# Kernel optimization log

Measured on AMD Instinct MI355X. Metric: run time of the kernel, lower is better.

The kernel has to match this reference:

```python
import jax, jax.numpy as jnp
import numpy as np

EPS = 1e-5  # torch BatchNorm2d default
Q_SHIFT = 2.0 ** 10   # deci_w = 10
Q_UPPER = 2.0 ** 15   # 2**(deci_w + inte_w) with inte_w = 5


def quantize(a):
    # emulate torch: (a*shift).int() truncates toward zero, clamp, rescale
    q = jnp.trunc(a * Q_SHIFT)
    q = jnp.clip(q, -Q_UPPER, Q_UPPER)
    return q / Q_SHIFT


def bn_train(x, gamma, beta):
    # training-mode BatchNorm2d: biased batch stats over (N, T, V)
    m = x.mean(axis=(0, 2, 3), keepdims=True)
    v = x.var(axis=(0, 2, 3), keepdims=True)
    return (x - m) * jax.lax.rsqrt(v + EPS) * gamma[None, :, None, None] + beta[None, :, None, None]


def setup_inputs() -> dict:
    key = jax.random.key(0)
    ks = jax.random.split(key, 8)
    N, C, T, V, S, K = 64, 64, 300, 25, 3, 9
    x = jax.random.normal(ks[0], (N, C, T, V), jnp.float32)
    A = jax.random.uniform(ks[1], (S, V, V), jnp.float32)
    PA = jax.random.normal(ks[2], (S, V, V), jnp.float32) * 1e-6
    # conv_d: 1x1 convs, (subset, out_ch, in_ch); conv_branch_init scale
    Wd = jax.random.normal(ks[3], (S, C, C), jnp.float32) * np.sqrt(2.0 / (C * S)).astype(np.float32)
    bd = jax.random.normal(ks[4], (S, C), jnp.float32) * 0.01
    gamma1 = jnp.ones((C,), jnp.float32)
    beta1 = jnp.zeros((C,), jnp.float32)
    # temporal 9x1 conv (out_ch, in_ch, K)
    Wt = jax.random.normal(ks[5], (C, C, K), jnp.float32) * np.sqrt(2.0 / (C * K)).astype(np.float32)
    bt = jnp.zeros((C,), jnp.float32)
    gamma2 = jnp.ones((C,), jnp.float32)
    beta2 = jnp.zeros((C,), jnp.float32)
    return {"x": x, "A": A, "PA": PA, "Wd": Wd, "bd": bd,
            "gamma1": gamma1, "beta1": beta1,
            "Wt": Wt, "bt": bt, "gamma2": gamma2, "beta2": beta2}


def reference(x, A, PA, Wd, bd, gamma1, beta1, Wt, bt, gamma2, beta2):
    # --- unit_gcn (prune_switch path, serial<=0, use_ck=False) ---
    Aq = jax.lax.stop_gradient(quantize(A + PA))  # quantize runs under no_grad
    num_subset = A.shape[0]
    z = None
    for s in range(num_subset):  # fixed small structural loop (3 subsets)
        xa = jnp.einsum('nctv,vw->nctw', x, Aq[s])          # graph matmul over V
        zs = jnp.einsum('nctv,oc->notv', xa, Wd[s]) + bd[s][None, :, None, None]  # 1x1 conv
        z = zs if z is None else z + zs
    y = bn_train(z, gamma1, beta1) + x  # down is identity (in==out)
    y = jax.nn.relu(y)
    # --- unit_tcn: 9x1 temporal conv, pad 4, stride 1, then BN ---
    out = jax.lax.conv_general_dilated(
        y, Wt[..., None], window_strides=(1, 1), padding=((4, 4), (0, 0)),
        dimension_numbers=('NCHW', 'OIHW', 'NCHW')) + bt[None, :, None, None]
    out = bn_train(out, gamma2, beta2)
    # --- residual (identity) + ReLU ---
    return jax.nn.relu(out + x)
```

## Files before the change

### kernel.cpp

```cpp
#include <hip/hip_runtime.h>

#define NB 64
#define CB 64
#define TB 300
#define VB 25
#define SB 3
#define KB 9
#define NCNTF 480000.0f

#define WS_SUM1 0
#define WS_SQ1  64
#define WS_SC1  128
#define WS_SH1  192
#define WS_SUM2 256
#define WS_SQ2  320
#define WS_SC2  384
#define WS_SH2  448
#define WS_WTP_BYTE 2048
#define WS_AQP_BYTE 75776
#define WS_WDP_BYTE 88064
#define WS_TC_BYTE  262144
#define ZP_ELEMS    30720000

typedef __attribute__((ext_vector_type(8))) short short8v;
typedef __attribute__((ext_vector_type(4))) float f32x4;
typedef __attribute__((ext_vector_type(16))) float f32x16;

__device__ __forceinline__ float bf2f(unsigned short u) {
  unsigned int v = ((unsigned int)u) << 16;
  float f; __builtin_memcpy(&f, &v, 4); return f;
}
__device__ __forceinline__ unsigned short f2bf(float f) {
  unsigned int x; __builtin_memcpy(&x, &f, 4);
  x += 0x7fffu + ((x >> 16) & 1u);
  return (unsigned short)(x >> 16);
}

__global__ void k0_prep(const float* __restrict__ A, const float* __restrict__ PA,
                        const float* __restrict__ Wd, const float* __restrict__ Wt,
                        float* __restrict__ ws) {
  int gid = blockIdx.x * 256 + threadIdx.x;
  int gs  = gridDim.x * 256;
  for (int i = gid; i < 512; i += gs) ws[i] = 0.f;
  unsigned short* wtp = (unsigned short*)((char*)ws + WS_WTP_BYTE);
  for (int idx = gid; idx < 36*2*64*8; idx += gs) {
    int j = idx & 7, li = (idx >> 3) & 63, mt = (idx >> 9) & 1, kt = idx >> 10;
    int o = mt*32 + (li & 31);
    int i = (kt & 3)*16 + (li >> 5)*8 + j;
    int tap = kt >> 2;
    wtp[idx] = f2bf(Wt[(o*64 + i)*9 + tap]);
  }
  unsigned short* aqp = (unsigned short*)((char*)ws + WS_AQP_BYTE);
  for (int idx = gid; idx < 12*64*8; idx += gs) {
    int j = idx & 7, l = (idx >> 3) & 63, fi = idx >> 9;
    int h = fi & 1, wt = (fi >> 1) & 1, s = fi >> 2;
    int v = (l >> 4)*8 + j, w = wt*16 + (l & 15);
    unsigned short out = 0;
    if (v < VB && w < VB) {
      int ai = (s*VB + v)*VB + w;
      float a = A[ai] + PA[ai];
      float q = truncf(a * 1024.f);
      q = fminf(fmaxf(q, -32768.f), 32768.f);
      float aq = q * (1.f/1024.f);
      unsigned short hi = f2bf(aq);
      out = h ? f2bf(aq - bf2f(hi)) : hi;
    }
    aqp[idx] = out;
  }
  unsigned short* wdp = (unsigned short*)((char*)ws + WS_WDP_BYTE);
  for (int idx = gid; idx < 48*64*8; idx += gs) {
    int j = idx & 7, l = (idx >> 3) & 63, fi = idx >> 9;
    int mt = fi & 3, q2 = fi >> 2;
    int kt = q2 % 6, h = q2 / 6;
    int k = kt*32 + (l >> 4)*8 + j;
    int s = k >> 6, c = k & 63, o = mt*16 + (l & 15);
    float wv = Wd[(s*64 + o)*64 + c];
    unsigned short hi = f2bf(wv);
    wdp[idx] = h ? f2bf(wv - bf2f(hi)) : hi;
  }
}

__global__ __launch_bounds__(512, 4) void k1_gcn(
    const float* __restrict__ x, const float* __restrict__ bd,
    const float* __restrict__ ws, float* __restrict__ wstat,
    unsigned short* __restrict__ zout, unsigned short* __restrict__ xtout)
{
  __shared__ __align__(16) char k1lds[52000];
  __shared__ float s_sum[CB], s_sq[CB];
  unsigned short* xtl = (unsigned short*)k1lds;
  char*  xab = k1lds + 26400;
  float* zg  = (float*)k1lds;
  int tid = threadIdx.x;
  int t0 = blockIdx.x * 8;
  int n  = blockIdx.y;
  int wv = tid >> 6, l = tid & 63, r = l & 15, g = l >> 4;
  int lim = 7500 - t0*25; if (lim > 200) lim = 200;

  if (tid < CB) { s_sum[tid] = 0.f; s_sq[tid] = 0.f; }

  for (int idx4 = tid; idx4 < 3200; idx4 += 512) {
    int c = idx4 / 50, q = idx4 - c*50;
    int tv0 = q*4;
    if (tv0 + 4 <= lim) {
      float4 xv = *(const float4*)(x + (size_t)(n*64 + c)*7500 + t0*25 + tv0);
      xtl[(tv0+0)*66 + c] = f2bf(xv.x);
      xtl[(tv0+1)*66 + c] = f2bf(xv.y);
      xtl[(tv0+2)*66 + c] = f2bf(xv.z);
      xtl[(tv0+3)*66 + c] = f2bf(xv.w);
    }
  }
  __syncthreads();

  short8v b1[4];
  #pragma unroll
  for (int ct = 0; ct < 4; ++ct) {
    int c = ct*16 + r;
    #pragma unroll
    for (int j = 0; j < 8; ++j) {
      int v = g*8 + j;
      b1[ct][j] = (v < VB) ? (short)xtl[(wv*25 + v)*66 + c] : (short)0;
    }
  }
  for (int idx = tid; idx < 12800; idx += 512) {
    int tv = idx >> 6, c = idx & 63;
    if (tv < lim)
      xtout[n*480000 + t0*1600 + idx] = xtl[tv*66 + c];
  }

  const unsigned short* aqp = (const unsigned short*)((const char*)ws + WS_AQP_BYTE);
  const unsigned short* wdp = (const unsigned short*)((const char*)ws + WS_WDP_BYTE);
  int mt2 = wv & 3, th2 = wv >> 2;
  f32x4 acc2[7];
  #pragma unroll
  for (int i = 0; i < 7; ++i) acc2[i] = (f32x4){0.f,0.f,0.f,0.f};

  for (int s = 0; s < SB; ++s) {
    #pragma unroll
    for (int wt = 0; wt < 2; ++wt) {
      short8v a1h = *(const short8v*)(aqp + ((s*4 + wt*2 + 0)*64 + l)*8);
      short8v a1l = *(const short8v*)(aqp + ((s*4 + wt*2 + 1)*64 + l)*8);
      f32x4 acc1[4];
      #pragma unroll
      for (int ct = 0; ct < 4; ++ct) acc1[ct] = (f32x4){0.f,0.f,0.f,0.f};
      #pragma unroll
      for (int ct = 0; ct < 4; ++ct) {
        acc1[ct] = __builtin_amdgcn_mfma_f32_16x16x32_bf16(a1h, b1[ct], acc1[ct], 0,0,0);
        acc1[ct] = __builtin_amdgcn_mfma_f32_16x16x32_bf16(a1l, b1[ct], acc1[ct], 0,0,0);
      }
      #pragma unroll
      for (int ct = 0; ct < 4; ++ct)
        #pragma unroll
        for (int reg = 0; reg < 4; ++reg) {
          int w = wt*16 + g*4 + reg;
          if (w < VB) {
            int row = wv*25 + w, c = ct*16 + r;
            int bir = (c*2) ^ ((row & 7) << 4);
            *(unsigned short*)(xab + row*128 + bir) = f2bf(acc1[ct][reg]);
          }
        }
    }
    __syncthreads();
    #pragma unroll
    for (int ktl = 0; ktl < 2; ++ktl) {
      int kt = s*2 + ktl;
      short8v ah = *(const short8v*)(wdp + ((kt*4 + mt2)*64 + l)*8);
      short8v al = *(const short8v*)(wdp + (((6 + kt)*4 + mt2)*64 + l)*8);
      #pragma unroll
      for (int ctl = 0; ctl < 7; ++ctl) {
        int rowb = th2*112 + ctl*16 + r;
        if (rowb > 199) rowb = 199;
        int bir = (ktl*64 + g*16) ^ ((rowb & 7) << 4);
        short8v b = *(const short8v*)(xab + rowb*128 + bir);
        acc2[ctl] = __builtin_amdgcn_mfma_f32_16x16x32_bf16(ah, b, acc2[ctl], 0,0,0);
        acc2[ctl] = __builtin_amdgcn_mfma_f32_16x16x32_bf16(al, b, acc2[ctl], 0,0,0);
      }
    }
    __syncthreads();
  }

  #pragma unroll
  for (int ctl = 0; ctl < 7; ++ctl) {
    int tw = th2*112 + ctl*16 + r;
    if (tw < 200) {
      #pragma unroll
      for (int reg = 0; reg < 4; ++reg)
        zg[tw*65 + mt2*16 + g*4 + reg] = acc2[ctl][reg];
    }
  }
  __syncthreads();

  {
    int o = tid & 63, chunk = tid >> 6;
    float bsum = bd[o] + bd[CB + o] + bd[2*CB + o];
    unsigned short* zr = zout + n*480000 + t0*1600 + o;
    float sm = 0.f, sq = 0.f;
    for (int qq = 0; qq < 25; ++qq) {
      int tw = chunk*25 + qq;
      if (tw < lim) {
        float val = zg[tw*65 + o] + bsum;
        zr[tw*64] = f2bf(val);
        sm += val; sq += val*val;
      }
    }
    atomicAdd(&s_sum[o], sm);
    atomicAdd(&s_sq[o], sq);
  }
  __syncthreads();
  if (tid < CB) {
    atomicAdd(&wstat[WS_SUM1 + tid], s_sum[tid]);
    atomicAdd(&wstat[WS_SQ1  + tid], s_sq[tid]);
  }
}

__global__ void k_fin(const float* __restrict__ g, const float* __restrict__ b,
                      float* __restrict__ ws, int soff) {
  int c = threadIdx.x;
  float m   = ws[soff + c] * (1.f/NCNTF);
  float var = ws[soff + 64 + c] * (1.f/NCNTF) - m*m;
  float rstd = rsqrtf(var + 1e-5f);
  float sc = rstd * g[c];
  ws[soff + 128 + c] = sc;
  ws[soff + 192 + c] = b[c] - m * sc;
}

__global__ __launch_bounds__(512, 4) void k3_mfma(
    const unsigned short* __restrict__ zb, const unsigned short* __restrict__ xtb,
    const float* __restrict__ bt, const float* __restrict__ ws,
    float* __restrict__ wstat, unsigned short* __restrict__ tco)
{
  __shared__ __align__(16) char ubuf[52480];
  __shared__ float s_sum[CB], s_sq[CB];
  int tid = threadIdx.x;
  int t0 = blockIdx.x * 8;
  int n  = blockIdx.y;
  int wv = tid >> 6, l = tid & 63;
  int lane31 = l & 31, lh = l >> 5;
  int mt = wv & 1, cth = wv >> 1;

  if (tid < CB) { s_sum[tid] = 0.f; s_sq[tid] = 0.f; }

  {
    int c0 = (tid & 15) * 4;
    int rowsel = tid >> 4;
    float4 sc4 = *(const float4*)(ws + WS_SC1 + c0);
    float4 sh4 = *(const float4*)(ws + WS_SH1 + c0);
    for (int it = 0; it < 13; ++it) {
      int tv = it*32 + rowsel;
      if (tv < 400) {
        int gt = t0 - 4 + tv/25;
        ushort4 yv = {0,0,0,0};
        if (gt >= 0 && gt < TB) {
          int addr = n*480000 + (t0-4)*1600 + tv*64 + c0;
          ushort4 z4 = *(const ushort4*)(zb + addr);
          ushort4 x4 = *(const ushort4*)(xtb + addr);
          yv.x = f2bf(fmaxf(fmaf(bf2f(z4.x), sc4.x, sh4.x) + bf2f(x4.x), 0.f));
          yv.y = f2bf(fmaxf(fmaf(bf2f(z4.y), sc4.y, sh4.y) + bf2f(x4.y), 0.f));
          yv.z = f2bf(fmaxf(fmaf(bf2f(z4.z), sc4.z, sh4.z) + bf2f(x4.z), 0.f));
          yv.w = f2bf(fmaxf(fmaf(bf2f(z4.w), sc4.w, sh4.w) + bf2f(x4.w), 0.f));
        }
        int wb = (tv << 7) + ((c0*2) ^ ((tv & 7) << 4));
        *(ushort4*)(ubuf + wb) = yv;
      }
    }
  }
  __syncthreads();

  const unsigned short* wtp = (const unsigned short*)((const char*)ws + WS_WTP_BYTE);
  f32x16 acc0, acc1;
  #pragma unroll
  for (int i = 0; i < 16; ++i) { acc0[i]=0.f; acc1[i]=0.f; }

  for (int ph = 0; ph < 2; ++ph) {
    short8v af[18];
    #pragma unroll
    for (int q = 0; q < 18; ++q)
      af[q] = *(const short8v*)(wtp + (((ph*18 + q)*2 + mt)*64 + l)*8);
    #pragma unroll
    for (int q = 0; q < 18; ++q) {
      int kt = ph*18 + q;
      int tap = kt >> 2;
      int ioff2 = ((kt & 3)*16 + lh*8) * 2;
#define DOCT(ACC, CTL) { \
      int col = (cth*2 + (CTL))*32 + lane31; \
      int tvB = (col < 200 ? col : 199) + 25*tap; \
      int ab = (tvB << 7) + (ioff2 ^ ((tvB & 7) << 4)); \
      short8v b = *(const short8v*)(ubuf + ab); \
      ACC = __builtin_amdgcn_mfma_f32_32x32x16_bf16(af[q], b, ACC, 0, 0, 0); }
      DOCT(acc0, 0) DOCT(acc1, 1)
#undef DOCT
    }
  }
  __syncthreads();

  float* tcl = (float*)ubuf;
  {
    int rowbase = mt*32 + 4*lh;
#define STCT(ACC, CTL) { \
    int col = (cth*2 + (CTL))*32 + lane31; \
    if (col < 200) { \
      _Pragma("unroll") \
      for (int rg = 0; rg < 16; ++rg) { \
        int o = rowbase + (rg & 3) + 8*(rg >> 2); \
        tcl[o*205 + col] = ACC[rg]; } } }
    STCT(acc0, 0) STCT(acc1, 1)
#undef STCT
  }
  __syncthreads();

  int lim = 7500 - t0*25; if (lim > 200) lim = 200;
  {
    int o = tid & 63, ch = tid >> 6;
    float bto = bt[o];
    float sm = 0.f, sq = 0.f;
    for (int q = 0; q < 25; ++q) {
      int tv = ch*25 + q;
      if (tv < lim) {
        float val = tcl[o*205 + tv] + bto;
        sm += val; sq += val*val;
      }
    }
    atomicAdd(&s_sum[o], sm);
    atomicAdd(&s_sq[o], sq);
  }
  {
    for (int oo = 0; oo < 8; ++oo) {
      int o2 = wv*8 + oo;
      float bto2 = bt[o2];
      unsigned short* tr = tco + n*480000 + o2*7500 + t0*25;
      #pragma unroll
      for (int sub = 0; sub < 2; ++sub) {
        int tv2 = (sub*64 + l)*2;
        if (tv2 < lim) {
          ushort2 pk;
          pk.x = f2bf(tcl[o2*205 + tv2] + bto2);
          pk.y = f2bf(tcl[o2*205 + tv2 + 1] + bto2);
          *(ushort2*)(tr + tv2) = pk;
        }
      }
    }
  }
  __syncthreads();
  if (tid < CB) {
    atomicAdd(&wstat[WS_SUM2 + tid], s_sum[tid]);
    atomicAdd(&wstat[WS_SQ2  + tid], s_sq[tid]);
  }
}

__global__ __launch_bounds__(256) void k5_final(
    const float* __restrict__ x, const float* __restrict__ ws,
    const unsigned short* __restrict__ tc, float* __restrict__ out)
{
  int idx = blockIdx.x * blockDim.x + threadIdx.x;
  int stride = gridDim.x * blockDim.x;
  const int total4 = NB*CB*TB*VB/4;
  for (int i = idx; i < total4; i += stride) {
    int c = (i / 1875) & 63;
    float sc = ws[WS_SC2 + c], sh = ws[WS_SH2 + c];
    ushort4 t4 = ((const ushort4*)tc)[i];
    float4  x4 = ((const float4*)x)[i];
    float4 r;
    r.x = fmaxf(fmaf(bf2f(t4.x), sc, sh) + x4.x, 0.f);
    r.y = fmaxf(fmaf(bf2f(t4.y), sc, sh) + x4.y, 0.f);
    r.z = fmaxf(fmaf(bf2f(t4.z), sc, sh) + x4.z, 0.f);
    r.w = fmaxf(fmaf(bf2f(t4.w), sc, sh) + x4.w, 0.f);
    ((float4*)out)[i] = r;
  }
}

extern "C" void kernel_launch(void* const* d_in, const int* in_sizes, int n_in,
                              void* d_out, int out_size, void* d_ws, size_t ws_size,
                              hipStream_t stream) {
  const float* x  = (const float*)d_in[0];
  const float* A  = (const float*)d_in[1];
  const float* PA = (const float*)d_in[2];
  const float* Wd = (const float*)d_in[3];
  const float* bd = (const float*)d_in[4];
  const float* g1 = (const float*)d_in[5];
  const float* b1 = (const float*)d_in[6];
  const float* Wt = (const float*)d_in[7];
  const float* bt = (const float*)d_in[8];
  const float* g2 = (const float*)d_in[9];
  const float* b2 = (const float*)d_in[10];

  float* ws = (float*)d_ws;
  unsigned short* zbuf = (unsigned short*)d_out;
  unsigned short* xtb  = (unsigned short*)d_out + ZP_ELEMS;
  unsigned short* tc   = (unsigned short*)((char*)d_ws + WS_TC_BYTE);
  float* out = (float*)d_out;

  k0_prep<<<dim3(64), dim3(256), 0, stream>>>(A, PA, Wd, Wt, ws);
  k1_gcn<<<dim3(38, 64), dim3(512), 0, stream>>>(x, bd, ws, ws, zbuf, xtb);
  k_fin<<<dim3(1), dim3(64), 0, stream>>>(g1, b1, ws, 0);
  k3_mfma<<<dim3(38, 64), dim3(512), 0, stream>>>(zbuf, xtb, bt, ws, ws, tc);
  k_fin<<<dim3(1), dim3(64), 0, stream>>>(g2, b2, ws, 256);
  k5_final<<<dim3(2048), dim3(256), 0, stream>>>(x, ws, tc, out);
}
```

Baseline: 291.7 us.

## Halve k1 LDS footprint by aliasing buffers and staging output in two halves

Shrinks the k1_gcn shared-memory buffer from about 52KB to 26.4KB. The xab staging area now aliases the xtl region, which needs an extra barrier, and the fp32 output tile is written out in two 100-row halves instead of all 200 rows at once. The aim is to let more 512-thread blocks stay resident per CU, raising occupancy. The cost is more __syncthreads and a serialized two-phase writeback.

```diff
diff --git a/kernel.cpp b/kernel.cpp
--- a/kernel.cpp
+++ b/kernel.cpp
@@ -85,11 +85,11 @@
     const float* __restrict__ ws, float* __restrict__ wstat,
     unsigned short* __restrict__ zout, unsigned short* __restrict__ xtout)
 {
-  __shared__ __align__(16) char k1lds[52000];
+  __shared__ __align__(16) char k1lds[26400];
   __shared__ float s_sum[CB], s_sq[CB];
   unsigned short* xtl = (unsigned short*)k1lds;
-  char*  xab = k1lds + 26400;
-  float* zg  = (float*)k1lds;
+  char*  xab = k1lds;
+  float* zgh = (float*)k1lds;
   int tid = threadIdx.x;
   int t0 = blockIdx.x * 8;
   int n  = blockIdx.y;
@@ -126,6 +126,7 @@
     if (tv < lim)
       xtout[n*480000 + t0*1600 + idx] = xtl[tv*66 + c];
   }
+  __syncthreads();
 
   const unsigned short* aqp = (const unsigned short*)((const char*)ws + WS_AQP_BYTE);
   const unsigned short* wdp = (const unsigned short*)((const char*)ws + WS_WDP_BYTE);
@@ -178,32 +179,72 @@
     __syncthreads();
   }
 
-  #pragma unroll
-  for (int ctl = 0; ctl < 7; ++ctl) {
-    int tw = th2*112 + ctl*16 + r;
-    if (tw < 200) {
+  float bsum, smv = 0.f, sqv = 0.f;
+  {
+    int o = tid & 63;
+    bsum = bd[o] + bd[CB + o] + bd[2*CB + o];
+  }
+  if (th2 == 0) {
+    #pragma unroll
+    for (int ctl = 0; ctl < 7; ++ctl) {
+      int tw = ctl*16 + r;
+      if (tw < 100) {
+        #pragma unroll
+        for (int reg = 0; reg < 4; ++reg)
+          zgh[tw*65 + mt2*16 + g*4 + reg] = acc2[ctl][reg];
+      }
+    }
+  }
+  __syncthreads();
+  {
+    int o = tid & 63, ch = tid >> 6;
+    unsigned short* zr = zout + n*480000 + t0*1600 + o;
+    for (int q = 0; q < 13; ++q) {
+      int y = ch*13 + q;
+      if (y < 100 && y < lim) {
+        float val = zgh[y*65 + o] + bsum;
+        zr[y*64] = f2bf(val);
+        smv += val; sqv += val*val;
+      }
+    }
+  }
+  __syncthreads();
+  if (th2 == 0) {
+    int tw = 6*16 + r;
+    if (tw >= 100) {
       #pragma unroll
       for (int reg = 0; reg < 4; ++reg)
-        zg[tw*65 + mt2*16 + g*4 + reg] = acc2[ctl][reg];
-    }
-  }
-  __syncthreads();
-
-  {
-    int o = tid & 63, chunk = tid >> 6;
-    float bsum = bd[o] + bd[CB + o] + bd[2*CB + o];
+        zgh[(tw-100)*65 + mt2*16 + g*4 + reg] = acc2[6][reg];
+    }
+  } else {
+    #pragma unroll
+    for (int ctl = 0; ctl < 6; ++ctl) {
+      int tw = 112 + ctl*16 + r;
+      if (tw < 200) {
+        #pragma unroll
+        for (int reg = 0; reg < 4; ++reg)
+          zgh[(tw-100)*65 + mt2*16 + g*4 + reg] = acc2[ctl][reg];
+      }
+    }
+  }
+  __syncthreads();
+  {
+    int o = tid & 63, ch = tid >> 6;
     unsigned short* zr = zout + n*480000 + t0*1600 + o;
-    float sm = 0.f, sq = 0.f;
-    for (int qq = 0; qq < 25; ++qq) {
-      int tw = chunk*25 + qq;
-      if (tw < lim) {
-        float val = zg[tw*65 + o] + bsum;
+    for (int q = 0; q < 13; ++q) {
+      int y = ch*13 + q;
+      int tw = 100 + y;
+      if (y < 100 && tw < lim) {
+        float val = zgh[tw*65 - 100*65 + o] + bsum;
         zr[tw*64] = f2bf(val);
-        sm += val; sq += val*val;
-      }
-    }
-    atomicAdd(&s_sum[o], sm);
-    atomicAdd(&s_sq[o], sq);
+        smv += val; sqv += val*val;
+      }
+    }
+  }
+  {
+    int o = tid & 63;
+    atomicAdd(&s_sum[o], smv);
+    atomicAdd(&s_sq[o], sqv);
   }
   __syncthreads();
   if (tid < CB) {
```

After: 297.2 us. About the same (+1.9%).
